# Optimization experiments

Measured on AMD Instinct MI355X. Metric: run time of the kernel, lower is better.

The kernel has to match this reference:

```python
import jax, jax.numpy as jnp
import numpy as np

B, S, D, V = 2, 4096, 2048, 32000
H, HD = 16, 128          # heads, head dim (H*HD == D)
BS = 16                  # block_size
N_ANCH = 128             # num_anchors (static: loss_mask=ones guarantees enough valid positions)
MASK_ID = 31999
DFF = 8192


def rms(x, w, eps=1e-6):
    return x * jax.lax.rsqrt(jnp.mean(x * x, axis=-1, keepdims=True) + eps) * w


def rope(x, pos):
    # x: (..., L, H, hd), pos: (..., L)
    hd = x.shape[-1]
    inv = 1.0 / (10000.0 ** (jnp.arange(0, hd, 2, dtype=jnp.float32) / hd))
    ang = pos[..., None, None].astype(jnp.float32) * inv  # (..., L, 1, hd/2)
    cos, sin = jnp.cos(ang), jnp.sin(ang)
    x1, x2 = x[..., : hd // 2], x[..., hd // 2 :]
    return jnp.concatenate([x1 * cos - x2 * sin, x2 * cos + x1 * sin], axis=-1).astype(x.dtype)


def setup_inputs() -> dict:
    key = jax.random.key(0)
    ks = jax.random.split(key, 12)
    s = 0.02
    return {
        "input_ids": jax.random.randint(ks[0], (B, S), 0, V, dtype=jnp.int32),
        "hidden_states": jax.random.normal(ks[1], (B, S, D), dtype=jnp.float32),
        "loss_mask": jnp.ones((B, S), dtype=jnp.float32),
        "rand_vals": jax.random.uniform(ks[2], (B, S - BS + 1), dtype=jnp.float32),
        "embed_table": jax.random.normal(ks[3], (V, D), dtype=jnp.float32) * s,
        "lm_head_w": jax.random.normal(ks[4], (V, D), dtype=jnp.float32) * s,
        "wq": jax.random.normal(ks[5], (D, D), dtype=jnp.float32) * s,
        "wk": jax.random.normal(ks[6], (D, D), dtype=jnp.float32) * s,
        "wv": jax.random.normal(ks[7], (D, D), dtype=jnp.float32) * s,
        "wo": jax.random.normal(ks[8], (D, D), dtype=jnp.float32) * s,
        "w_gate": jax.random.normal(ks[9], (D, DFF), dtype=jnp.float32) * s,
        "w_up": jax.random.normal(ks[10], (D, DFF), dtype=jnp.float32) * s,
        "w_down": jax.random.normal(ks[11], (DFF, D), dtype=jnp.float32) * s,
        "norm_attn": jnp.ones((D,), dtype=jnp.float32),
        "norm_mlp": jnp.ones((D,), dtype=jnp.float32),
        "norm_out": jnp.ones((D,), dtype=jnp.float32),
        "norm_chs": jnp.ones((D,), dtype=jnp.float32),
    }


def reference(input_ids, hidden_states, loss_mask, rand_vals, embed_table, lm_head_w,
              wq, wk, wv, wo, w_gate, w_up, w_down, norm_attn, norm_mlp, norm_out, norm_chs):
    max_anchor = S - BS
    # ---- anchor sampling: random permutation of valid positions via argsort of rand ----
    valid = loss_mask[:, : max_anchor + 1] > 0.5                       # (B, max_anchor+1)
    valid_counts = valid.sum(axis=1)
    idx = jnp.arange(max_anchor + 1, dtype=jnp.int32)
    masked_idx = jnp.where(valid, idx[None, :], S + 1)
    rv = jnp.where(valid, rand_vals, 2.0)
    order = jnp.argsort(rv, axis=1)
    gathered = jnp.take_along_axis(masked_idx, order, axis=1)
    anchors = jnp.sort(gathered[:, :N_ANCH], axis=1)                   # (B, N)
    keep = jnp.arange(N_ANCH)[None, :] < jnp.minimum(valid_counts, N_ANCH)[:, None]
    anchors = jnp.where(keep, anchors, 0)
    # ---- noise embedding: anchor token at block start, mask token elsewhere ----
    anchor_tok = jnp.take_along_axis(input_ids, jnp.clip(anchors, 0, S - 1), axis=1)
    first_tok = jnp.where(keep, anchor_tok, MASK_ID)
    noise_ids = jnp.full((B, N_ANCH, BS), MASK_ID, dtype=jnp.int32).at[:, :, 0].set(first_tok)
    x = embed_table[noise_ids]                                         # (B,N,BS,D)
    # ---- CHS context hidden: target hidden at anchor-1 ----
    ctx_pos = jnp.maximum(anchors - 1, 0)
    ctx = jnp.take_along_axis(hidden_states, ctx_pos[:, :, None], axis=1)  # (B,N,D)
    # ---- block-diagonal attention: per-block kv = [CHS_i | draft block i] (kv_len=1+BS) ----
    pos_q = anchors[:, :, None] + jnp.arange(BS)[None, None, :]        # (B,N,BS)
    pos_kv = jnp.concatenate([ctx_pos[:, :, None], pos_q], axis=2)     # (B,N,1+BS)
    hq = rms(x, norm_attn)
    hc = rms(ctx, norm_chs)[:, :, None, :]
    kv_in = jnp.concatenate([hc, hq], axis=2)                          # (B,N,1+BS,D)
    q = rope((hq @ wq).reshape(B, N_ANCH, BS, H, HD), pos_q)
    k = rope((kv_in @ wk).reshape(B, N_ANCH, 1 + BS, H, HD), pos_kv)
    v = (kv_in @ wv).reshape(B, N_ANCH, 1 + BS, H, HD)
    scores = jnp.einsum('bnqhd,bnkhd->bnhqk', q, k) * (1.0 / HD ** 0.5)
    attn = jax.nn.softmax(scores, axis=-1)
    out = jnp.einsum('bnhqk,bnkhd->bnqhd', attn, v).reshape(B, N_ANCH, BS, D) @ wo
    out = out * keep[:, :, None, None].astype(out.dtype)               # invalid blocks fully masked
    x = x + out
    h = rms(x, norm_mlp)
    x = x + (jax.nn.silu(h @ w_gate) * (h @ w_up)) @ w_down
    h_out = rms(x, norm_out)
    logits = h_out @ lm_head_w.T                                       # (B,N,BS,V)
    # ---- block-wise CE loss ----
    label_idx = anchors[:, :, None] + jnp.arange(BS)[None, None, :]
    valid_label = label_idx < S
    safe = jnp.minimum(label_idx, S - 1)
    targets = jnp.take_along_axis(jnp.broadcast_to(input_ids[:, None, :], (B, N_ANCH, S)), safe, axis=2)
    lm_g = jnp.take_along_axis(jnp.broadcast_to(loss_mask[:, None, :], (B, N_ANCH, S)), safe, axis=2)
    weight = (keep[:, :, None] & valid_label).astype(jnp.float32)
    weight = weight * (jnp.arange(BS) > 0)[None, None, :].astype(jnp.float32) * lm_g
    logp = jax.nn.log_softmax(logits, axis=-1)
    tok_logp = jnp.take_along_axis(logp, targets[..., None].astype(jnp.int32), axis=-1)[..., 0]
    loss = -(tok_logp * weight).sum() / (weight.sum() + 1e-6)
    pred = jnp.argmax(logits, axis=-1)
    accuracy = ((pred == targets) & (weight > 0.5)).sum().astype(jnp.float32) / (weight.sum() + 1e-6)
    return loss, accuracy
```

## Files before the change

kernel.cpp:

```cpp
#include <hip/hip_runtime.h>
#include <math.h>

typedef unsigned short u16;
typedef unsigned char u8;
typedef short v8s __attribute__((ext_vector_type(8)));
typedef u16   v4u __attribute__((ext_vector_type(4)));
typedef float v4f __attribute__((ext_vector_type(4)));
typedef int   v2i __attribute__((ext_vector_type(2)));
typedef int   v4i __attribute__((ext_vector_type(4)));

#define DEVFN static __device__ __forceinline__

constexpr int cB = 2, cS = 4096, cD = 2048, cV = 32000, cH = 16, cHD = 128;
constexpr int cBS = 16, cNA = 128, cMASK = 31999, cDFF = 8192;
constexpr int NCAND = cS - cBS + 1;
constexpr int MTOK  = cB * cNA * cBS;
constexpr int MKV   = cB * cNA * 17;
constexpr int NCH   = cV / 128;
constexpr int NCH2  = cV / 256;

constexpr int EPI_BF16 = 0, EPI_SILU = 1, EPI_OEMB = 2, EPI_DOWNACC = 3, EPI_STATS = 4;
constexpr int ASRC_BF16 = 0, ASRC_RMS = 1, ASRC_AOMAP = 2;

struct RmsSrc {
  const float* hs; const float* emb; const float* nattn; const float* nchs;
  const float* rowinv; const int* ftok; const int* cpos;
};

DEVFN u16 f2bf(float f) {
  union { float f; unsigned u; } a; a.f = f;
  unsigned u = a.u;
  u = u + 0x7fffu + ((u >> 16) & 1u);
  return (u16)(u >> 16);
}
DEVFN float bf2f(u16 h) {
  union { unsigned u; float f; } a; a.u = ((unsigned)h) << 16;
  return a.f;
}
DEVFN float waveSum(float v) {
  #pragma unroll
  for (int o = 32; o >= 1; o >>= 1) v += __shfl_xor(v, o);
  return v;
}
DEVFN void gload16(void* lds, const void* g) {
  __builtin_amdgcn_global_load_lds(
      (const __attribute__((address_space(1))) unsigned*)g,
      (__attribute__((address_space(3))) unsigned*)lds, 16, 0, 0);
}
DEVFN int pack4fp8(float a, float b, float c, float d) {
  int p = __builtin_amdgcn_cvt_pk_fp8_f32(a, b, 0, 0);
  p = __builtin_amdgcn_cvt_pk_fp8_f32(c, d, p, 1);
  return p;
}
DEVFN long perm8(long i) {
  return (i & ~63L) | (((i >> 3) & 3) << 4) | (((i >> 5) & 1) << 3);
}

__global__ void k_select(const float* __restrict__ lmask, const float* __restrict__ rv_in,
                         int* __restrict__ self) {
  int b = blockIdx.x >> 4, chunk = blockIdx.x & 15;
  __shared__ float rvs[4096];
  for (int i = threadIdx.x; i < NCAND; i += 256) {
    bool valid = lmask[(size_t)b * cS + i] > 0.5f;
    rvs[i] = valid ? rv_in[(size_t)b * NCAND + i] : 2.0f;
  }
  __syncthreads();
  int i = chunk * 256 + threadIdx.x;
  if (i < NCAND) {
    float v = rvs[i];
    int rank = 0;
    for (int j = 0; j < NCAND; ++j) {
      float u = rvs[j];
      rank += (u < v) || (u == v && j < i);
    }
    self[(size_t)b * NCAND + i] = (rank < cNA) ? 1 : 0;
  }
}

__global__ void k_anchors(const float* __restrict__ lmask, const int* __restrict__ self,
                          const int* __restrict__ ids, int* __restrict__ anchors,
                          int* __restrict__ keepA, int* __restrict__ ftok, int* __restrict__ cpos) {
  int b = blockIdx.x;
  __shared__ int flags[4096];
  __shared__ int ssum[256];
  __shared__ int soff[257];
  __shared__ int abuf[cNA];
  for (int i = threadIdx.x; i < 4096; i += 256)
    flags[i] = (i < NCAND) ? (self[(size_t)b * NCAND + i] && (lmask[(size_t)b * cS + i] > 0.5f)) : 0;
  if (threadIdx.x < cNA) abuf[threadIdx.x] = 0;
  __syncthreads();
  int s = 0;
  #pragma unroll
  for (int j = 0; j < 16; ++j) s += flags[threadIdx.x * 16 + j];
  ssum[threadIdx.x] = s;
  __syncthreads();
  if (threadIdx.x == 0) {
    int a = 0;
    for (int t = 0; t < 256; ++t) { soff[t] = a; a += ssum[t]; }
    soff[256] = a;
  }
  __syncthreads();
  int nsel = soff[256];
  int p = soff[threadIdx.x];
  for (int j = 0; j < 16; ++j) {
// ... 38 lines not shown
                         const int* __restrict__ ftok, const int* __restrict__ cpos,
                         u16* __restrict__ kv) {
  int r = blockIdx.x;
  int j = r % 17, bn = r / 17, b = bn >> 7;
  const float* src; const float* w;
  if (j == 0) { src = hs + ((size_t)b * cS + cpos[bn]) * cD; w = nchs; }
  else {
    int tok = (j == 1) ? ftok[bn] : cMASK;
    src = emb + (size_t)tok * cD; w = nattn;
  }
  float ss = 0.f;
  for (int d = threadIdx.x; d < cD; d += 256) { float v = src[d]; ss += v * v; }
  ss = waveSum(ss);
  __shared__ float red[4];
  if ((threadIdx.x & 63) == 0) red[threadIdx.x >> 6] = ss;
  __syncthreads();
  float tot = red[0] + red[1] + red[2] + red[3];
  float inv = 1.0f / sqrtf(tot / cD + 1e-6f);
  for (int d = threadIdx.x; d < cD; d += 256)
    kv[(size_t)r * cD + d] = f2bf(src[d] * inv * w[d]);
}

__global__ void k_rms(const float* __restrict__ xin, const float* __restrict__ w,
                      u16* __restrict__ outp) {
  int m = blockIdx.x;
  const float* row = xin + (size_t)m * cD;
  float ss = 0.f;
  for (int d = threadIdx.x; d < cD; d += 256) { float v = row[d]; ss += v * v; }
  ss = waveSum(ss);
  __shared__ float red[4];
  if ((threadIdx.x & 63) == 0) red[threadIdx.x >> 6] = ss;
  __syncthreads();
  float tot = red[0] + red[1] + red[2] + red[3];
  float inv = 1.0f / sqrtf(tot / cD + 1e-6f);
  for (int d = threadIdx.x; d < cD; d += 256)
    outp[(size_t)m * cD + d] = f2bf(row[d] * inv * w[d]);
}

__global__ void k_conv8(const float* __restrict__ in, u8* __restrict__ out, long n, float scale) {
  long i = ((long)blockIdx.x * 256 + threadIdx.x) * 8;
  long stride = (long)gridDim.x * 256 * 8;
  for (; i < n; i += stride) {
    v4f a = *(const v4f*)(in + i), b = *(const v4f*)(in + i + 4);
    v2i pk;
    pk[0] = pack4fp8(a[0] * scale, a[1] * scale, a[2] * scale, a[3] * scale);
    pk[1] = pack4fp8(b[0] * scale, b[1] * scale, b[2] * scale, b[3] * scale);
    *(v2i*)(out + perm8(i)) = pk;
  }
}

__global__ void k_cvt8(const u16* __restrict__ in, u8* __restrict__ out, long n) {
  long i = ((long)blockIdx.x * 256 + threadIdx.x) * 8;
  long stride = (long)gridDim.x * 256 * 8;
  for (; i < n; i += stride) {
    v8s a = *(const v8s*)(in + i);
    v2i pk;
    pk[0] = pack4fp8(bf2f((u16)a[0]), bf2f((u16)a[1]), bf2f((u16)a[2]), bf2f((u16)a[3]));
    pk[1] = pack4fp8(bf2f((u16)a[4]), bf2f((u16)a[5]), bf2f((u16)a[6]), bf2f((u16)a[7]));
    *(v2i*)(out + perm8(i)) = pk;
  }
}

__global__ void k_tconv(const float* __restrict__ W, u16* __restrict__ WT, int K, int N) {
  __shared__ u16 t[64][72];
  int n0 = blockIdx.x * 64, k0 = blockIdx.y * 64;
  int tid = threadIdx.x;
  int c4 = (tid & 15) * 4, r0 = tid >> 4;
  #pragma unroll
  for (int rr = 0; rr < 64; rr += 16) {
    int k = r0 + rr;
    v4f v = *(const v4f*)(W + (size_t)(k0 + k) * N + n0 + c4);
    #pragma unroll
    for (int e = 0; e < 4; ++e) t[c4 + e][k] = f2bf(v[e]);
  }
  __syncthreads();
  int n = tid >> 2, kq = (tid & 3) * 16;
  v8s o0, o1;
  #pragma unroll
  for (int e = 0; e < 8; ++e) { o0[e] = (short)t[n][kq + e]; o1[e] = (short)t[n][kq + 8 + e]; }
  *(v8s*)(WT + (size_t)(n0 + n) * K + k0 + kq) = o0;
  *(v8s*)(WT + (size_t)(n0 + n) * K + k0 + kq + 8) = o1;
}

template <int EPI>
__launch_bounds__(512, 1)
__global__ void k_gemm6(const u16* __restrict__ Abf, const u16* __restrict__ Bbf,
                        u16* __restrict__ Cbf, const u16* __restrict__ Gaux,
                        v4f* __restrict__ partials, int K, int ldc, int nch) {
  __shared__ __align__(16) u16 lds[65536];
  const int tid = threadIdx.x;
  const int lane = tid & 63, wid = tid >> 6;
  const int wm = wid >> 2, wn = wid & 3;
  const int lc = lane & 15, lq = lane >> 4;
  const int m0 = blockIdx.x * 256, n0 = blockIdx.y * 256;

  const u16* srcA[2]; const u16* srcB[2];
  #pragma unroll
  for (int i = 0; i < 2; ++i) {
    int s = i * 512 + tid;
    int row = s >> 2;
    int c2 = (s & 3) ^ ((row >> 1) & 3);
    srcA[i] = Abf + (size_t)(m0 + row) * K + c2 * 8;
    srcB[i] = Bbf + (size_t)(n0 + row) * K + c2 * 8;
  }

  v4f acc[8][4];
  #pragma unroll
  for (int i = 0; i < 8; ++i)
    #pragma unroll
    for (int j = 0; j < 4; ++j) acc[i][j] = (v4f){0.f, 0.f, 0.f, 0.f};

  const int fsw = lq ^ ((lc >> 1) & 3);
  int aoff[8], boff[4];
  #pragma unroll
  for (int mi = 0; mi < 8; ++mi) aoff[mi] = ((wm * 128 + mi * 16 + lc) * 4 + fsw) * 8;
  #pragma unroll
  for (int ni = 0; ni < 4; ++ni) boff[ni] = ((wn * 64 + ni * 16 + lc) * 4 + fsw) * 8;

  auto stageA = [&](int t, int kh) {
    int reg = (t & 1) * 32768 + kh * 8192;
    int koff = t * 64 + kh * 32;
    #pragma unroll
    for (int i = 0; i < 2; ++i)
      gload16(&lds[reg + i * 4096 + wid * 512], srcA[i] + koff);
  };
  auto stageB = [&](int t, int kh) {
    int reg = (t & 1) * 32768 + 16384 + kh * 8192;
    int koff = t * 64 + kh * 32;
    #pragma unroll
    for (int i = 0; i < 2; ++i)
      gload16(&lds[reg + i * 4096 + wid * 512], srcB[i] + koff);
  };

  stageA(0, 0); stageB(0, 0);
  stageA(0, 1); stageB(0, 1);
  stageA(1, 0); stageB(1, 0);
  asm volatile("s_waitcnt vmcnt(8)" ::: "memory");
  __builtin_amdgcn_s_barrier();

  const int NT = K >> 6;
  for (int t = 0; t < NT; ++t) {
    const int bufb = (t & 1) * 32768;
    const u16* Ab0 = &lds[bufb];
    const u16* Ab1 = &lds[bufb + 8192];
    const u16* Bb0 = &lds[bufb + 16384];
    const u16* Bb1 = &lds[bufb + 24576];
    v8s a_[4], b_[4];

    #pragma unroll
    for (int ni = 0; ni < 4; ++ni) b_[ni] = *(const v8s*)(Bb0 + boff[ni]);
    #pragma unroll
    for (int mi = 0; mi < 4; ++mi) a_[mi] = *(const v8s*)(Ab0 + aoff[mi]);
    if (t + 1 < NT) stageA(t + 1, 1);
    asm volatile("s_waitcnt lgkmcnt(0)" ::: "memory");
    __builtin_amdgcn_sched_barrier(0);
    __builtin_amdgcn_s_setprio(1);
    #pragma unroll
    for (int mi = 0; mi < 4; ++mi)
      #pragma unroll
      for (int ni = 0; ni < 4; ++ni)
        acc[mi][ni] = __builtin_amdgcn_mfma_f32_16x16x32_bf16(a_[mi], b_[ni], acc[mi][ni], 0, 0, 0);
    __builtin_amdgcn_s_setprio(0);
    __builtin_amdgcn_s_barrier();

    #pragma unroll
    for (int mi = 0; mi < 4; ++mi) a_[mi] = *(const v8s*)(Ab0 + aoff[mi + 4]);
    if (t + 1 < NT) stageB(t + 1, 1);
    asm volatile("s_waitcnt lgkmcnt(0)" ::: "memory");
    __builtin_amdgcn_sched_barrier(0);
    __builtin_amdgcn_s_setprio(1);
    #pragma unroll
    for (int mi = 0; mi < 4; ++mi)
      #pragma unroll
      for (int ni = 0; ni < 4; ++ni)
        acc[mi + 4][ni] = __builtin_amdgcn_mfma_f32_16x16x32_bf16(a_[mi], b_[ni], acc[mi + 4][ni], 0, 0, 0);
    __builtin_amdgcn_s_setprio(0);
    if (t + 1 < NT) { asm volatile("s_waitcnt vmcnt(4)" ::: "memory"); }
    else            { asm volatile("s_waitcnt vmcnt(0)" ::: "memory"); }
    __builtin_amdgcn_s_barrier();

    #pragma unroll
    for (int ni = 0; ni < 4; ++ni) b_[ni] = *(const v8s*)(Bb1 + boff[ni]);
    #pragma unroll
    for (int mi = 0; mi < 4; ++mi) a_[mi] = *(const v8s*)(Ab1 + aoff[mi]);
    if (t + 2 < NT) stageA(t + 2, 0);
    asm volatile("s_waitcnt lgkmcnt(0)" ::: "memory");
    __builtin_amdgcn_sched_barrier(0);
    __builtin_amdgcn_s_setprio(1);
    #pragma unroll
    for (int mi = 0; mi < 4; ++mi)
      #pragma unroll
      for (int ni = 0; ni < 4; ++ni)
        acc[mi][ni] = __builtin_amdgcn_mfma_f32_16x16x32_bf16(a_[mi], b_[ni], acc[mi][ni], 0, 0, 0);
    __builtin_amdgcn_s_setprio(0);
    __builtin_amdgcn_s_barrier();

    #pragma unroll
    for (int mi = 0; mi < 4; ++mi) a_[mi] = *(const v8s*)(Ab1 + aoff[mi + 4]);
    if (t + 2 < NT) stageB(t + 2, 0);
    asm volatile("s_waitcnt lgkmcnt(0)" ::: "memory");
    __builtin_amdgcn_sched_barrier(0);
    __builtin_amdgcn_s_setprio(1);
    #pragma unroll
    for (int mi = 0; mi < 4; ++mi)
      #pragma unroll
      for (int ni = 0; ni < 4; ++ni)
        acc[mi + 4][ni] = __builtin_amdgcn_mfma_f32_16x16x32_bf16(a_[mi], b_[ni], acc[mi + 4][ni], 0, 0, 0);
    __builtin_amdgcn_s_setprio(0);
    __builtin_amdgcn_s_barrier();
  }
  asm volatile("s_waitcnt vmcnt(0)" ::: "memory");

  #pragma unroll
  for (int mi = 0; mi < 8; ++mi)
    #pragma unroll
    for (int ni = 0; ni < 4; ++ni)
      #pragma unroll
      for (int r = 0; r < 4; ++r) {
        int grow = m0 + wm * 128 + mi * 16 + lq * 4 + r;
        int gcol = n0 + wn * 64 + ni * 16 + lc;
        size_t idx = (size_t)grow * ldc + gcol;
        float vv = acc[mi][ni][r];
        if constexpr (EPI == EPI_BF16) {
          Cbf[idx] = f2bf(vv);
        } else {
          float g = bf2f(Gaux[idx]);
          Cbf[idx] = f2bf(vv * g / (1.0f + __expf(-g)));
        }
      }
  (void)partials; (void)nch;
}

__launch_bounds__(512, 2)
__global__ void k_gemm8(const u8* __restrict__ A8, const u8* __restrict__ B8,
                        v4f* __restrict__ partials, int K, int nch) {
  __shared__ __align__(16) u8 lds8[65536];
  const int tid = threadIdx.x;
  const int lane = tid & 63, wid = tid >> 6;
  const int wm = wid >> 2, wn = wid & 3;
  const int lc = lane & 15, lq = lane >> 4;
  const int m0 = blockIdx.x * 256, n0 = blockIdx.y * 256;

  const u8* srcA[2]; const u8* srcB[2];
  #pragma unroll
  for (int i = 0; i < 2; ++i) {
    int ci = i * 512 + tid;
    int r = ci >> 2;
    int logc = (ci & 3) ^ ((r >> 1) & 3);
    srcA[i] = A8 + (size_t)(m0 + r) * K + logc * 16;
    srcB[i] = B8 + (size_t)(n0 + r) * K + logc * 16;
  }

  v4f acc[8][4];
  #pragma unroll
  for (int i = 0; i < 8; ++i)
    #pragma unroll
    for (int j = 0; j < 4; ++j) acc[i][j] = (v4f){0.f, 0.f, 0.f, 0.f};

  const int csw = (lc >> 1) & 3;
  int aoff[8], boff[4];
  #pragma unroll
  for (int mi = 0; mi < 8; ++mi) aoff[mi] = (wm * 128 + mi * 16 + lc) * 64 + ((lq ^ csw) << 4);
  #pragma unroll
  for (int ni = 0; ni < 4; ++ni) boff[ni] = (wn * 64 + ni * 16 + lc) * 64 + ((lq ^ csw) << 4);

  auto stageA = [&](int t, int i) {
    gload16(&lds8[(t & 1) * 32768 + i * 8192 + wid * 1024], srcA[i] + t * 64);
  };
  auto stageB = [&](int t, int i) {
    gload16(&lds8[(t & 1) * 32768 + 16384 + i * 8192 + wid * 1024], srcB[i] + t * 64);
  };

  stageA(0, 0); stageA(0, 1); stageB(0, 0); stageB(0, 1);
  stageA(1, 0); stageA(1, 1); stageB(1, 0); stageB(1, 1);
  asm volatile("s_waitcnt vmcnt(4)" ::: "memory");
  __builtin_amdgcn_s_barrier();

  union Frag { v4i v; long long ll[2]; };
  const int NT = K >> 6;
  for (int t = 0; t < NT; ++t) {
    const u8* Ab = &lds8[(t & 1) * 32768];
    const u8* Bb = Ab + 16384;
    Frag fa[8], fb[4];

    #pragma unroll
    for (int ni = 0; ni < 4; ++ni) fb[ni].v = *(const v4i*)(Bb + boff[ni]);
    #pragma unroll
    for (int mi = 0; mi < 4; ++mi) fa[mi].v = *(const v4i*)(Ab + aoff[mi]);
    asm volatile("s_waitcnt lgkmcnt(0)" ::: "memory");
    __builtin_amdgcn_sched_barrier(0);
    __builtin_amdgcn_s_setprio(1);
    #pragma unroll
    for (int mi = 0; mi < 4; ++mi)
      #pragma unroll
      for (int ni = 0; ni < 4; ++ni)
        acc[mi][ni] = __builtin_amdgcn_mfma_f32_16x16x32_fp8_fp8(fa[mi].ll[0], fb[ni].ll[0], acc[mi][ni], 0, 0, 0);
    __builtin_amdgcn_s_setprio(0);
    __builtin_amdgcn_s_barrier();

    #pragma unroll
    for (int mi = 0; mi < 4; ++mi) fa[mi + 4].v = *(const v4i*)(Ab + aoff[mi + 4]);
    if (t + 2 < NT) stageB(t + 2, 0);
    asm volatile("s_waitcnt lgkmcnt(0)" ::: "memory");
    __builtin_amdgcn_sched_barrier(0);
    __builtin_amdgcn_s_setprio(1);
    #pragma unroll
    for (int mi = 0; mi < 4; ++mi)
      #pragma unroll
      for (int ni = 0; ni < 4; ++ni)
        acc[mi + 4][ni] = __builtin_amdgcn_mfma_f32_16x16x32_fp8_fp8(fa[mi + 4].ll[0], fb[ni].ll[0], acc[mi + 4][ni], 0, 0, 0);
    __builtin_amdgcn_s_setprio(0);
    __builtin_amdgcn_s_barrier();

    if (t + 2 < NT) { stageB(t + 2, 1); stageA(t + 2, 0); }
    __builtin_amdgcn_s_setprio(1);
    #pragma unroll
    for (int mi = 0; mi < 4; ++mi)
      #pragma unroll
      for (int ni = 0; ni < 4; ++ni)
        acc[mi][ni] = __builtin_amdgcn_mfma_f32_16x16x32_fp8_fp8(fa[mi].ll[1], fb[ni].ll[1], acc[mi][ni], 0, 0, 0);
    __builtin_amdgcn_s_setprio(0);
    __builtin_amdgcn_s_barrier();

    if (t + 2 < NT) stageA(t + 2, 1);
    __builtin_amdgcn_s_setprio(1);
    #pragma unroll
    for (int mi = 0; mi < 4; ++mi)
      #pragma unroll
      for (int ni = 0; ni < 4; ++ni)
        acc[mi + 4][ni] = __builtin_amdgcn_mfma_f32_16x16x32_fp8_fp8(fa[mi + 4].ll[1], fb[ni].ll[1], acc[mi + 4][ni], 0, 0, 0);
    __builtin_amdgcn_s_setprio(0);
    if (t + 2 < NT) { asm volatile("s_waitcnt vmcnt(4)" ::: "memory"); }
    else            { asm volatile("s_waitcnt vmcnt(0)" ::: "memory"); }
    __builtin_amdgcn_s_barrier();
  }
  asm volatile("s_waitcnt vmcnt(0)" ::: "memory");

  #pragma unroll
  for (int mi = 0; mi < 8; ++mi)
    #pragma unroll
    for (int ni = 0; ni < 4; ++ni)
      acc[mi][ni] *= 0.015625f;

  float* s_mx = (float*)lds8;
  float* s_sm = (float*)(lds8 + 4096);
  int*   s_ax = (int*)(lds8 + 8192);
  __syncthreads();
  #pragma unroll
  for (int mi = 0; mi < 8; ++mi) {
    #pragma unroll
    for (int r = 0; r < 4; ++r) {
      float v0 = acc[mi][0][r], v1 = acc[mi][1][r], v2 = acc[mi][2][r], v3 = acc[mi][3][r];
      float mx = v0; int ax = lc;
      if (v1 > mx) { mx = v1; ax = 16 + lc; }
      if (v2 > mx) { mx = v2; ax = 32 + lc; }
      if (v3 > mx) { mx = v3; ax = 48 + lc; }
      #pragma unroll
      for (int off = 1; off < 16; off <<= 1) {
        float om = __shfl_xor(mx, off); int oa = __shfl_xor(ax, off);
        if (om > mx || (om == mx && oa < ax)) { mx = om; ax = oa; }
      }
      float se = __expf(v0 - mx) + __expf(v1 - mx) + __expf(v2 - mx) + __expf(v3 - mx);
      #pragma unroll
      for (int off = 1; off < 16; off <<= 1) se += __shfl_xor(se, off);
      if (lc == 0) {
        int row = wm * 128 + mi * 16 + lq * 4 + r;
        s_mx[row * 4 + wn] = mx; s_sm[row * 4 + wn] = se; s_ax[row * 4 + wn] = wn * 64 + ax;
      }
    }
  }
  __syncthreads();
  if (tid < 256) {
    float gm = s_mx[tid * 4]; int ga = s_ax[tid * 4];
    #pragma unroll
    for (int w = 1; w < 4; ++w) {
      float m = s_mx[tid * 4 + w];
      if (m > gm) { gm = m; ga = s_ax[tid * 4 + w]; }
    }
    float gs = 0.f;
    #pragma unroll
    for (int w = 0; w < 4; ++w) gs += s_sm[tid * 4 + w] * __expf(s_mx[tid * 4 + w] - gm);
    v4f rec; rec[0] = gm; rec[1] = gs; rec[2] = __int_as_float(n0 + ga); rec[3] = 0.f;
    partials[(size_t)(m0 + tid) * nch + blockIdx.y] = rec;
  }
}

template <int ASRC, int EPI>
__launch_bounds__(256, 2)
__global__ void k_gemm4(const u16* __restrict__ Abf, const u16* __restrict__ Bbf,
                        u16* __restrict__ Cbf, float* __restrict__ Cf32,
                        const int* __restrict__ keepArr, RmsSrc rs, int K, int ldb, int ldc) {
  __shared__ __align__(16) u16 lds[2][16384];
  const int tid = threadIdx.x;
  const int lane = tid & 63, wid = tid >> 6;
  const int wm = wid >> 1, wn = wid & 1;
  const int lc = lane & 15, lq = lane >> 4;
  const int m0 = blockIdx.x * 128, n0 = blockIdx.y * 128;

  const u16* srcA[4]; const u16* srcB[4];
  #pragma unroll
  for (int i = 0; i < 4; ++i) {
    int s = i * 256 + tid;
    int row = s >> 3;
    int c3 = (s & 7) ^ (row & 7);
    int ar = m0 + row;
    if constexpr (ASRC == ASRC_AOMAP) ar = (ar >> 4) * 17 + 1 + (ar & 15);
    srcA[i] = Abf + (size_t)ar * K + c3 * 8;
    srcB[i] = Bbf + (size_t)(n0 + row) * ldb + c3 * 8;
  }

  v4f acc[4][4];
  #pragma unroll
  for (int i = 0; i < 4; ++i)
    #pragma unroll
    for (int j = 0; j < 4; ++j) acc[i][j] = (v4f){0.f, 0.f, 0.f, 0.f};

  const int sw = lc & 7;
  const int aoff0 = (((wm * 64 + lc) * 8 + 0 + lq) ^ sw) * 8;
  const int aoff1 = (((wm * 64 + lc) * 8 + 4 + lq) ^ sw) * 8;
  const int boff0 = (((wn * 64 + lc) * 8 + 0 + lq) ^ sw) * 8;
  const int boff1 = (((wn * 64 + lc) * 8 + 4 + lq) ^ sw) * 8;

  auto stageTo = [&](int b) {
    u16* dA = &lds[b][0] + wid * 512;
    u16* dB = &lds[b][8192] + wid * 512;
    #pragma unroll
    for (int i = 0; i < 4; ++i) { gload16(dA + i * 2048, srcA[i]); srcA[i] += 64; }
    #pragma unroll
    for (int i = 0; i < 4; ++i) { gload16(dB + i * 2048, srcB[i]); srcB[i] += 64; }
  };

  stageTo(0);
  const int NT = K >> 6;
  for (int t = 0; t < NT; ++t) {
    const int cur = t & 1;
    if (t + 1 < NT) {
      stageTo(cur ^ 1);
      asm volatile("s_waitcnt vmcnt(8)" ::: "memory");
    } else {
      asm volatile("s_waitcnt vmcnt(0)" ::: "memory");
    }
    __builtin_amdgcn_s_barrier();
    const u16* Ab = &lds[cur][0];
    const u16* Bb = &lds[cur][8192];
    v8s a0[4], a1[4], b0[4], b1[4];
    #pragma unroll
    for (int mi = 0; mi < 4; ++mi) a0[mi] = *(const v8s*)(Ab + aoff0 + mi * 1024);
    #pragma unroll
    for (int ni = 0; ni < 4; ++ni) b0[ni] = *(const v8s*)(Bb + boff0 + ni * 1024);
    #pragma unroll
    for (int mi = 0; mi < 4; ++mi) a1[mi] = *(const v8s*)(Ab + aoff1 + mi * 1024);
    #pragma unroll
    for (int ni = 0; ni < 4; ++ni) b1[ni] = *(const v8s*)(Bb + boff1 + ni * 1024);
    __builtin_amdgcn_s_setprio(1);
    #pragma unroll
    for (int mi = 0; mi < 4; ++mi)
      #pragma unroll
      for (int ni = 0; ni < 4; ++ni)
        acc[mi][ni] = __builtin_amdgcn_mfma_f32_16x16x32_bf16(a0[mi], b0[ni], acc[mi][ni], 0, 0, 0);
    __builtin_amdgcn_s_setprio(0);
    asm volatile("s_waitcnt lgkmcnt(0)" ::: "memory");
    __builtin_amdgcn_sched_barrier(0);
    __builtin_amdgcn_s_barrier();
    __builtin_amdgcn_s_setprio(1);
    #pragma unroll
    for (int mi = 0; mi < 4; ++mi)
// ... 328 lines not shown
__global__ void k_heartbeat(float* outp) {
  if (threadIdx.x == 0) { outp[0] = -55.0f; outp[1] = -55.0f; }
}
__global__ void k_sentinel(float* outp) {
  if (threadIdx.x == 0) { outp[0] = -777.0f; outp[1] = -777.0f; }
}

extern "C" void kernel_launch(void* const* d_in, const int* in_sizes, int n_in,
                              void* d_out, int out_size, void* d_ws, size_t ws_size,
                              hipStream_t stream) {
  const int*   ids   = (const int*)  d_in[0];
  const float* hs    = (const float*)d_in[1];
  const float* lmask = (const float*)d_in[2];
  const float* rv    = (const float*)d_in[3];
  const float* emb   = (const float*)d_in[4];
  const float* wlm   = (const float*)d_in[5];
  const float* wq    = (const float*)d_in[6];
  const float* wk    = (const float*)d_in[7];
  const float* wv    = (const float*)d_in[8];
  const float* wo    = (const float*)d_in[9];
  const float* wg    = (const float*)d_in[10];
  const float* wu    = (const float*)d_in[11];
  const float* wd    = (const float*)d_in[12];
  const float* nattn = (const float*)d_in[13];
  const float* nmlp  = (const float*)d_in[14];
  const float* nout  = (const float*)d_in[15];
  const float* nchs  = (const float*)d_in[16];
  (void)in_sizes; (void)n_in; (void)out_size;

  float* outp = (float*)d_out;
  k_heartbeat<<<dim3(1), 64, 0, stream>>>(outp);

  char* wsb = (char*)d_ws;
  size_t off = 0;
  auto alloc = [&](size_t bytes) -> void* {
    void* p = wsb + off;
    off = (off + bytes + 255) & ~(size_t)255;
    return p;
  };
  int*   anchors = (int*)  alloc((size_t)cB * cNA * 4);
  int*   keepA   = (int*)  alloc((size_t)cB * cNA * 4);
  int*   ftok    = (int*)  alloc((size_t)cB * cNA * 4);
  int*   cpos    = (int*)  alloc((size_t)cB * cNA * 4);
  int*   self    = (int*)  alloc((size_t)cB * NCAND * 4);
  float* rowinv  = (float*)alloc((size_t)MKV * 4);
  int*   ttok    = (int*)  alloc((size_t)MTOK * 4);
  float* tlogit  = (float*)alloc((size_t)MTOK * 4);
  float* tokOut  = (float*)alloc((size_t)MTOK * 4 * 4);

  const size_t szQ  = (size_t)MKV * cD * 2;
  const size_t szX  = (size_t)MTOK * cD * 4;
  u16* qb = (u16*)alloc(szQ);
  const size_t a1off = off;

  RmsSrc rs{hs, emb, nattn, nchs, rowinv, ftok, cpos};

  k_select <<<dim3(cB * 16), 256, 0, stream>>>(lmask, rv, self);
  k_anchors<<<dim3(cB),      256, 0, stream>>>(lmask, self, ids, anchors, keepA, ftok, cpos);

  const size_t szKV   = szQ;
  const size_t szCbuf = (size_t)MTOK * 4096 * 2;
  size_t kvb_off  = a1off;
  size_t a1f_off  = (kvb_off + szKV + 255) & ~(size_t)255;
  size_t a1f_sz   = 2 * szQ > (szX + szCbuf) ? 2 * szQ : (szX + szCbuf);
  size_t wreg_off = (a1f_off + a1f_sz + 255) & ~(size_t)255;
  size_t wreg_sz  = (size_t)cV * cD * 2;
  size_t need_fast = wreg_off + wreg_sz;

  if (need_fast <= ws_size) {
    u16*   kvb   = (u16*)(wsb + kvb_off);
    u16*   kb    = (u16*)(wsb + a1f_off);
    u16*   vb    = (u16*)(wsb + a1f_off + szQ);
    float* xb    = (float*)(wsb + a1f_off);
    u16*   cbuf  = (u16*)(wsb + a1f_off + szX);
    v4f*   parts = (v4f*)(wsb + a1f_off);
    u8*    h8    = (u8*)(wsb + a1f_off + (size_t)16 * 1024 * 1024);
    u16*   hb    = qb;
    u16*   houtb = qb;
    u16*   wT    = (u16*)(wsb + wreg_off);
    const size_t szDD = (size_t)cD * cD;
    u16* wqT = wT;            u16* wkT = wT + szDD;
    u16* wvT = wT + 2 * szDD; u16* woT = wT + 3 * szDD;
    const size_t szDF = (size_t)cD * cDFF;
    u16* wgT = wT; u16* wuT = wT + szDF; u16* wdT = wT + 2 * szDF;
    u8*  wlm8 = (u8*)wT;

    k_build2<<<dim3(MKV), 256, 0, stream>>>(hs, emb, nattn, nchs, ftok, cpos, kvb);

    k_tconv<<<dim3(32, 32), 256, 0, stream>>>(wq, wqT, cD, cD);
    k_tconv<<<dim3(32, 32), 256, 0, stream>>>(wk, wkT, cD, cD);
    k_tconv<<<dim3(32, 32), 256, 0, stream>>>(wv, wvT, cD, cD);
    k_tconv<<<dim3(32, 32), 256, 0, stream>>>(wo, woT, cD, cD);

    k_gemm4<ASRC_BF16, EPI_BF16><<<dim3(MKV / 128, cD / 128), 256, 0, stream>>>(
        kvb, wqT, qb, nullptr, nullptr, rs, cD, cD, cD);
    k_gemm4<ASRC_BF16, EPI_BF16><<<dim3(MKV / 128, cD / 128), 256, 0, stream>>>(
        kvb, wkT, kb, nullptr, nullptr, rs, cD, cD, cD);
    k_gemm4<ASRC_BF16, EPI_BF16><<<dim3(MKV / 128, cD / 128), 256, 0, stream>>>(
        kvb, wvT, vb, nullptr, nullptr, rs, cD, cD, cD);

    k_rope<<<dim3(2 * MKV), 256, 0, stream>>>(qb, kb, anchors, cpos);
    k_attn<<<dim3(cB * cNA * cH), 64, 0, stream>>>(qb, kb, vb);

    k_gemm4<ASRC_AOMAP, EPI_OEMB><<<dim3(MTOK / 128, cD / 128), 256, 0, stream>>>(
        qb, woT, nullptr, xb, keepA, rs, cD, cD, cD);

    k_rms<<<dim3(MTOK), 256, 0, stream>>>(xb, nmlp, hb);

    k_tconv<<<dim3(128, 32), 256, 0, stream>>>(wg, wgT, cD, cDFF);
    k_tconv<<<dim3(128, 32), 256, 0, stream>>>(wu, wuT, cD, cDFF);
    k_tconv<<<dim3(32, 128), 256, 0, stream>>>(wd, wdT, cDFF, cD);

    for (int cb = 0; cb < cDFF; cb += 4096) {
      k_gemm6<EPI_BF16><<<dim3(MTOK / 256, 16), 512, 0, stream>>>(
          hb, wgT + (size_t)cb * cD, cbuf, nullptr, nullptr, cD, 4096, 0);
      k_gemm6<EPI_SILU><<<dim3(MTOK / 256, 16), 512, 0, stream>>>(
          hb, wuT + (size_t)cb * cD, cbuf, cbuf, nullptr, cD, 4096, 0);
      k_gemm4<ASRC_BF16, EPI_DOWNACC><<<dim3(MTOK / 128, cD / 128), 256, 0, stream>>>(
          cbuf, wdT + cb, nullptr, xb, nullptr, rs, 4096, cDFF, cD);
    }

    k_rms<<<dim3(MTOK), 256, 0, stream>>>(xb, nout, houtb);

    k_tgt<<<dim3(MTOK / 4), 256, 0, stream>>>(houtb, wlm, ids, anchors, ttok, tlogit);

    k_cvt8 <<<dim3(1024), 256, 0, stream>>>(houtb, h8, (long)MTOK * cD);
    k_conv8<<<dim3(2048), 256, 0, stream>>>(wlm, wlm8, (long)cV * cD, 64.0f);
    k_gemm8<<<dim3(MTOK / 256, NCH2), 512, 0, stream>>>(h8, wlm8, parts, cD, NCH2);

    k_combine<<<dim3(MTOK), 256, 0, stream>>>(parts, ttok, tlogit, keepA, anchors, lmask, tokOut, NCH2);
    k_final  <<<dim3(1), 256, 0, stream>>>(tokOut, outp);
    return;
  }

  const int cwopts[4] = {4096, 2048, 1024, 512};
  int CW = 0;
  for (int ci = 0; ci < 4; ++ci) {
    int cw = cwopts[ci];
    size_t cbufsz = (size_t)MTOK * cw * 2;
    size_t s1 = 2 * szQ;
    size_t s2 = szX + cbufsz;
    size_t sz = s1 > s2 ? s1 : s2;
    size_t pmin = (size_t)MTOK * NCH * 16;
    if (pmin > sz) sz = pmin;
    if (a1off + sz <= ws_size) { CW = cw; break; }
  }
  if (CW == 0) { k_sentinel<<<dim3(1), 64, 0, stream>>>(outp); return; }

  u16*   kb    = (u16*)(wsb + a1off);
  u16*   vb    = (u16*)(wsb + a1off + szQ);
  float* xb    = (float*)(wsb + a1off);
  u16*   cbuf  = (u16*)(wsb + a1off + szX);
  v4f*   parts = (v4f*)(wsb + a1off);
  u16*   hb    = qb;
  u16*   houtb = qb;

  k_rowinv<<<dim3(MKV), 256, 0, stream>>>(hs, emb, ftok, cpos, rowinv);

  k_gemm<ASRC_RMS, 0, EPI_BF16><<<dim3(MKV / 128, cD / 128), 256, 0, stream>>>(
      nullptr, wq, qb, nullptr, nullptr, nullptr, nullptr, rs, cD, cD, cD);
  k_gemm<ASRC_RMS, 0, EPI_BF16><<<dim3(MKV / 128, cD / 128), 256, 0, stream>>>(
      nullptr, wk, kb, nullptr, nullptr, nullptr, nullptr, rs, cD, cD, cD);
  k_gemm<ASRC_RMS, 0, EPI_BF16><<<dim3(MKV / 128, cD / 128), 256, 0, stream>>>(
      nullptr, wv, vb, nullptr, nullptr, nullptr, nullptr, rs, cD, cD, cD);

  k_rope<<<dim3(2 * MKV), 256, 0, stream>>>(qb, kb, anchors, cpos);
  k_attn<<<dim3(cB * cNA * cH), 64, 0, stream>>>(qb, kb, vb);

  k_gemm<ASRC_AOMAP, 0, EPI_OEMB><<<dim3(MTOK / 128, cD / 128), 256, 0, stream>>>(
      qb, wo, nullptr, xb, nullptr, keepA, nullptr, rs, cD, cD, cD);

  k_rms<<<dim3(MTOK), 256, 0, stream>>>(xb, nmlp, hb);

  for (int cb = 0; cb < cDFF; cb += CW) {
    k_gemm<ASRC_BF16, 0, EPI_BF16><<<dim3(MTOK / 128, CW / 128), 256, 0, stream>>>(
        hb, wg + cb, cbuf, nullptr, nullptr, nullptr, nullptr, rs, cD, cDFF, CW);
    k_gemm<ASRC_BF16, 0, EPI_SILU><<<dim3(MTOK / 128, CW / 128), 256, 0, stream>>>(
        hb, wu + cb, cbuf, nullptr, cbuf, nullptr, nullptr, rs, cD, cDFF, CW);
    k_gemm<ASRC_BF16, 0, EPI_DOWNACC><<<dim3(MTOK / 128, cD / 128), 256, 0, stream>>>(
        cbuf, wd + (size_t)cb * cD, nullptr, xb, nullptr, nullptr, nullptr, rs, CW, cD, cD);
  }

  k_rms<<<dim3(MTOK), 256, 0, stream>>>(xb, nout, houtb);

  k_tgt<<<dim3(MTOK / 4), 256, 0, stream>>>(houtb, wlm, ids, anchors, ttok, tlogit);
  k_gemm<ASRC_BF16, 1, EPI_STATS><<<dim3(MTOK / 128, cV / 128), 256, 0, stream>>>(
      houtb, wlm, nullptr, nullptr, nullptr, nullptr, parts, rs, cD, cD, 0);

  k_combine<<<dim3(MTOK), 256, 0, stream>>>(parts, ttok, tlogit, keepA, anchors, lmask, tokOut, NCH);
  k_final  <<<dim3(1), 256, 0, stream>>>(tokOut, outp);
}
```

Baseline: 1.557 ms.

## Fuse gate/up GEMMs via interleaved weights and triple-buffer fp8 LM-head GEMM

```diff
diff --git a/kernel.cpp b/kernel.cpp
--- a/kernel.cpp
+++ b/kernel.cpp
@@ -19,7 +19,7 @@
 constexpr int NCH   = cV / 128;
 constexpr int NCH2  = cV / 256;
 
-constexpr int EPI_BF16 = 0, EPI_SILU = 1, EPI_OEMB = 2, EPI_DOWNACC = 3, EPI_STATS = 4;
+constexpr int EPI_BF16 = 0, EPI_SILU = 1, EPI_OEMB = 2, EPI_DOWNACC = 3, EPI_STATS = 4, EPI_GLU = 5;
 constexpr int ASRC_BF16 = 0, ASRC_RMS = 1, ASRC_AOMAP = 2;
 
 struct RmsSrc {
@@ -224,6 +224,29 @@
   *(v8s*)(WT + (size_t)(n0 + n) * K + k0 + kq + 8) = o1;
 }
 
+__global__ void k_tconv2(const float* __restrict__ W, u16* __restrict__ WT, int K, int N, int goff) {
+  __shared__ u16 t[64][72];
+  int n0 = blockIdx.x * 64, k0 = blockIdx.y * 64;
+  int tid = threadIdx.x;
+  int c4 = (tid & 15) * 4, r0 = tid >> 4;
+  #pragma unroll
+  for (int rr = 0; rr < 64; rr += 16) {
+    int k = r0 + rr;
+    v4f v = *(const v4f*)(W + (size_t)(k0 + k) * N + n0 + c4);
+    #pragma unroll
+    for (int e = 0; e < 4; ++e) t[c4 + e][k] = f2bf(v[e]);
+  }
+  __syncthreads();
+  int n = tid >> 2, kq = (tid & 3) * 16;
+  int gn = n0 + n;
+  size_t rout = ((size_t)(gn >> 4) << 5) + goff + (gn & 15);
+  v8s o0, o1;
+  #pragma unroll
+  for (int e = 0; e < 8; ++e) { o0[e] = (short)t[n][kq + e]; o1[e] = (short)t[n][kq + 8 + e]; }
+  *(v8s*)(WT + rout * K + k0 + kq) = o0;
+  *(v8s*)(WT + rout * K + k0 + kq + 8) = o1;
+}
+
 template <int EPI>
 __launch_bounds__(512, 1)
 __global__ void k_gemm6(const u16* __restrict__ Abf, const u16* __restrict__ Bbf,
@@ -353,30 +376,45 @@
   }
   asm volatile("s_waitcnt vmcnt(0)" ::: "memory");
 
-  #pragma unroll
-  for (int mi = 0; mi < 8; ++mi)
-    #pragma unroll
-    for (int ni = 0; ni < 4; ++ni)
-      #pragma unroll
-      for (int r = 0; r < 4; ++r) {
-        int grow = m0 + wm * 128 + mi * 16 + lq * 4 + r;
-        int gcol = n0 + wn * 64 + ni * 16 + lc;
-        size_t idx = (size_t)grow * ldc + gcol;
-        float vv = acc[mi][ni][r];
-        if constexpr (EPI == EPI_BF16) {
-          Cbf[idx] = f2bf(vv);
-        } else {
-          float g = bf2f(Gaux[idx]);
-          Cbf[idx] = f2bf(vv * g / (1.0f + __expf(-g)));
+  if constexpr (EPI == EPI_GLU) {
+    #pragma unroll
+    for (int mi = 0; mi < 8; ++mi)
+      #pragma unroll
+      for (int np = 0; np < 2; ++np)
+        #pragma unroll
+        for (int r = 0; r < 4; ++r) {
+          int grow = m0 + wm * 128 + mi * 16 + lq * 4 + r;
+          int gcol = (n0 >> 1) + wn * 32 + np * 16 + lc;
+          float g = acc[mi][2 * np][r];
+          float u = acc[mi][2 * np + 1][r];
+          Cbf[(size_t)grow * ldc + gcol] = f2bf(u * g / (1.0f + __expf(-g)));
         }
-      }
+  } else {
+    #pragma unroll
+    for (int mi = 0; mi < 8; ++mi)
+      #pragma unroll
+      for (int ni = 0; ni < 4; ++ni)
+        #pragma unroll
+        for (int r = 0; r < 4; ++r) {
+          int grow = m0 + wm * 128 + mi * 16 + lq * 4 + r;
+          int gcol = n0 + wn * 64 + ni * 16 + lc;
+          size_t idx = (size_t)grow * ldc + gcol;
+          float vv = acc[mi][ni][r];
+          if constexpr (EPI == EPI_BF16) {
+            Cbf[idx] = f2bf(vv);
+          } else {
+            float g = bf2f(Gaux[idx]);
+            Cbf[idx] = f2bf(vv * g / (1.0f + __expf(-g)));
+          }
+        }
+  }
   (void)partials; (void)nch;
 }
 
-__launch_bounds__(512, 2)
+__launch_bounds__(512, 1)
 __global__ void k_gemm8(const u8* __restrict__ A8, const u8* __restrict__ B8,
                         v4f* __restrict__ partials, int K, int nch) {
-  __shared__ __align__(16) u8 lds8[65536];
+  __shared__ __align__(16) u8 lds8[98304];
   const int tid = threadIdx.x;
   const int lane = tid & 63, wid = tid >> 6;
   const int wm = wid >> 2, wn = wid & 3;
@@ -406,22 +444,24 @@
   #pragma unroll
   for (int ni = 0; ni < 4; ++ni) boff[ni] = (wn * 64 + ni * 16 + lc) * 64 + ((lq ^ csw) << 4);
 
-  auto stageA = [&](int t, int i) {
-    gload16(&lds8[(t & 1) * 32768 + i * 8192 + wid * 1024], srcA[i] + t * 64);
+  auto stageA = [&](int buf, int t, int i) {
+    gload16(&lds8[buf * 32768 + i * 8192 + wid * 1024], srcA[i] + t * 64);
   };
-  auto stageB = [&](int t, int i) {
-    gload16(&lds8[(t & 1) * 32768 + 16384 + i * 8192 + wid * 1024], srcB[i] + t * 64);
+  auto stageB = [&](int buf, int t, int i) {
+    gload16(&lds8[buf * 32768 + 16384 + i * 8192 + wid * 1024], srcB[i] + t * 64);
   };
 
-  stageA(0, 0); stageA(0, 1); stageB(0, 0); stageB(0, 1);
-  stageA(1, 0); stageA(1, 1); stageB(1, 0); stageB(1, 1);
-  asm volatile("s_waitcnt vmcnt(4)" ::: "memory");
+  stageA(0, 0, 0); stageA(0, 0, 1); stageB(0, 0, 0); stageB(0, 0, 1);
+  stageA(1, 1, 0); stageA(1, 1, 1); stageB(1, 1, 0); stageB(1, 1, 1);
+  stageA(2, 2, 0); stageA(2, 2, 1); stageB(2, 2, 0); stageB(2, 2, 1);
+  asm volatile("s_waitcnt vmcnt(8)" ::: "memory");
   __builtin_amdgcn_s_barrier();
 
   union Frag { v4i v; long long ll[2]; };
   const int NT = K >> 6;
+  int cur = 0;
   for (int t = 0; t < NT; ++t) {
-    const u8* Ab = &lds8[(t & 1) * 32768];
+    const u8* Ab = &lds8[cur * 32768];
     const u8* Bb = Ab + 16384;
     Frag fa[8], fb[4];
 
@@ -442,7 +482,7 @@
 
     #pragma unroll
     for (int mi = 0; mi < 4; ++mi) fa[mi + 4].v = *(const v4i*)(Ab + aoff[mi + 4]);
-    if (t + 2 < NT) stageB(t + 2, 0);
+    if (t + 3 < NT) stageB(cur, t + 3, 0);
     asm volatile("s_waitcnt lgkmcnt(0)" ::: "memory");
     __builtin_amdgcn_sched_barrier(0);
     __builtin_amdgcn_s_setprio(1);
@@ -454,7 +494,7 @@
     __builtin_amdgcn_s_setprio(0);
     __builtin_amdgcn_s_barrier();
 
-    if (t + 2 < NT) { stageB(t + 2, 1); stageA(t + 2, 0); }
+    if (t + 3 < NT) { stageB(cur, t + 3, 1); stageA(cur, t + 3, 0); }
     __builtin_amdgcn_s_setprio(1);
     #pragma unroll
     for (int mi = 0; mi < 4; ++mi)
@@ -464,7 +504,7 @@
     __builtin_amdgcn_s_setprio(0);
     __builtin_amdgcn_s_barrier();
 
-    if (t + 2 < NT) stageA(t + 2, 1);
+    if (t + 3 < NT) stageA(cur, t + 3, 1);
     __builtin_amdgcn_s_setprio(1);
     #pragma unroll
     for (int mi = 0; mi < 4; ++mi)
@@ -472,9 +512,10 @@
       for (int ni = 0; ni < 4; ++ni)
         acc[mi + 4][ni] = __builtin_amdgcn_mfma_f32_16x16x32_fp8_fp8(fa[mi + 4].ll[1], fb[ni].ll[1], acc[mi + 4][ni], 0, 0, 0);
     __builtin_amdgcn_s_setprio(0);
-    if (t + 2 < NT) { asm volatile("s_waitcnt vmcnt(4)" ::: "memory"); }
+    if (t + 3 < NT) { asm volatile("s_waitcnt vmcnt(8)" ::: "memory"); }
     else            { asm volatile("s_waitcnt vmcnt(0)" ::: "memory"); }
     __builtin_amdgcn_s_barrier();
+    cur = (cur == 2) ? 0 : cur + 1;
   }
   asm volatile("s_waitcnt vmcnt(0)" ::: "memory");
 
@@ -1018,7 +1059,8 @@
     u16* wqT = wT;            u16* wkT = wT + szDD;
     u16* wvT = wT + 2 * szDD; u16* woT = wT + 3 * szDD;
     const size_t szDF = (size_t)cD * cDFF;
-    u16* wgT = wT; u16* wuT = wT + szDF; u16* wdT = wT + 2 * szDF;
+    u16* wguT = wT;
+    u16* wdT  = wT + 2 * szDF;
     u8*  wlm8 = (u8*)wT;
 
     k_build2<<<dim3(MKV), 256, 0, stream>>>(hs, emb, nattn, nchs, ftok, cpos, kvb);
@@ -1043,15 +1085,13 @@
 
     k_rms<<<dim3(MTOK), 256, 0, stream>>>(xb, nmlp, hb);
 
-    k_tconv<<<dim3(128, 32), 256, 0, stream>>>(wg, wgT, cD, cDFF);
-    k_tconv<<<dim3(128, 32), 256, 0, stream>>>(wu, wuT, cD, cDFF);
-    k_tconv<<<dim3(32, 128), 256, 0, stream>>>(wd, wdT, cDFF, cD);
+    k_tconv2<<<dim3(128, 32), 256, 0, stream>>>(wg, wguT, cD, cDFF, 0);
+    k_tconv2<<<dim3(128, 32), 256, 0, stream>>>(wu, wguT, cD, cDFF, 16);
+    k_tconv <<<dim3(32, 128), 256, 0, stream>>>(wd, wdT, cDFF, cD);
 
     for (int cb = 0; cb < cDFF; cb += 4096) {
-      k_gemm6<EPI_BF16><<<dim3(MTOK / 256, 16), 512, 0, stream>>>(
-          hb, wgT + (size_t)cb * cD, cbuf, nullptr, nullptr, cD, 4096, 0);
-      k_gemm6<EPI_SILU><<<dim3(MTOK / 256, 16), 512, 0, stream>>>(
-          hb, wuT + (size_t)cb * cD, cbuf, cbuf, nullptr, cD, 4096, 0);
+      k_gemm6<EPI_GLU><<<dim3(MTOK / 256, 32), 512, 0, stream>>>(
+          hb, wguT + (size_t)cb * 2 * cD, cbuf, nullptr, nullptr, cD, 4096, 0);
       k_gemm4<ASRC_BF16, EPI_DOWNACC><<<dim3(MTOK / 128, cD / 128), 256, 0, stream>>>(
           cbuf, wdT + cb, nullptr, xb, nullptr, rs, 4096, cDFF, cD);
     }
```

Result: no change. 1.545 ms (-0.7%).

## Fuse gate/up projections into one FP8 GEMM with SwiGLU epilogue

Applied to the files above, without the earlier changes.

```diff
diff --git a/kernel.cpp b/kernel.cpp
--- a/kernel.cpp
+++ b/kernel.cpp
@@ -19,7 +19,7 @@
 constexpr int NCH   = cV / 128;
 constexpr int NCH2  = cV / 256;
 
-constexpr int EPI_BF16 = 0, EPI_SILU = 1, EPI_OEMB = 2, EPI_DOWNACC = 3, EPI_STATS = 4;
+constexpr int EPI_BF16 = 0, EPI_SILU = 1, EPI_OEMB = 2, EPI_DOWNACC = 3, EPI_STATS = 4, EPI_GLU = 5;
 constexpr int ASRC_BF16 = 0, ASRC_RMS = 1, ASRC_AOMAP = 2;
 
 struct RmsSrc {
@@ -224,6 +224,33 @@
   *(v8s*)(WT + (size_t)(n0 + n) * K + k0 + kq + 8) = o1;
 }
 
+__global__ void k_tconv8(const float* __restrict__ W, u8* __restrict__ WT8,
+                         int K, int N, int goff, float scale) {
+  __shared__ float tf[64][65];
+  int n0 = blockIdx.x * 64, k0 = blockIdx.y * 64;
+  int tid = threadIdx.x;
+  int c4 = (tid & 15) * 4, r0 = tid >> 4;
+  #pragma unroll
+  for (int rr = 0; rr < 64; rr += 16) {
+    int k = r0 + rr;
+    v4f v = *(const v4f*)(W + (size_t)(k0 + k) * N + n0 + c4);
+    #pragma unroll
+    for (int e = 0; e < 4; ++e) tf[c4 + e][k] = v[e];
+  }
+  __syncthreads();
+  int n = tid >> 2, kq = (tid & 3) * 16;
+  int gn = n0 + n;
+  size_t rout = ((size_t)(gn >> 4) << 5) + goff + (gn & 15);
+  long base = (long)rout * K + k0 + kq;
+  v2i p0, p1;
+  p0[0] = pack4fp8(tf[n][kq + 0] * scale, tf[n][kq + 1] * scale, tf[n][kq + 2] * scale, tf[n][kq + 3] * scale);
+  p0[1] = pack4fp8(tf[n][kq + 4] * scale, tf[n][kq + 5] * scale, tf[n][kq + 6] * scale, tf[n][kq + 7] * scale);
+  p1[0] = pack4fp8(tf[n][kq + 8] * scale, tf[n][kq + 9] * scale, tf[n][kq + 10] * scale, tf[n][kq + 11] * scale);
+  p1[1] = pack4fp8(tf[n][kq + 12] * scale, tf[n][kq + 13] * scale, tf[n][kq + 14] * scale, tf[n][kq + 15] * scale);
+  *(v2i*)(WT8 + perm8(base)) = p0;
+  *(v2i*)(WT8 + perm8(base + 8)) = p1;
+}
+
 template <int EPI>
 __launch_bounds__(512, 1)
 __global__ void k_gemm6(const u16* __restrict__ Abf, const u16* __restrict__ Bbf,
@@ -353,29 +380,46 @@
   }
   asm volatile("s_waitcnt vmcnt(0)" ::: "memory");
 
-  #pragma unroll
-  for (int mi = 0; mi < 8; ++mi)
-    #pragma unroll
-    for (int ni = 0; ni < 4; ++ni)
-      #pragma unroll
-      for (int r = 0; r < 4; ++r) {
-        int grow = m0 + wm * 128 + mi * 16 + lq * 4 + r;
-        int gcol = n0 + wn * 64 + ni * 16 + lc;
-        size_t idx = (size_t)grow * ldc + gcol;
-        float vv = acc[mi][ni][r];
-        if constexpr (EPI == EPI_BF16) {
-          Cbf[idx] = f2bf(vv);
-        } else {
-          float g = bf2f(Gaux[idx]);
-          Cbf[idx] = f2bf(vv * g / (1.0f + __expf(-g)));
+  if constexpr (EPI == EPI_GLU) {
+    #pragma unroll
+    for (int mi = 0; mi < 8; ++mi)
+      #pragma unroll
+      for (int np = 0; np < 2; ++np)
+        #pragma unroll
+        for (int r = 0; r < 4; ++r) {
+          int grow = m0 + wm * 128 + mi * 16 + lq * 4 + r;
+          int gcol = (n0 >> 1) + wn * 32 + np * 16 + lc;
+          float g = acc[mi][2 * np][r];
+          float u = acc[mi][2 * np + 1][r];
+          Cbf[(size_t)grow * ldc + gcol] = f2bf(u * g / (1.0f + __expf(-g)));
         }
-      }
+  } else {
+    #pragma unroll
+    for (int mi = 0; mi < 8; ++mi)
+      #pragma unroll
+      for (int ni = 0; ni < 4; ++ni)
+        #pragma unroll
+        for (int r = 0; r < 4; ++r) {
+          int grow = m0 + wm * 128 + mi * 16 + lq * 4 + r;
+          int gcol = n0 + wn * 64 + ni * 16 + lc;
+          size_t idx = (size_t)grow * ldc + gcol;
+          float vv = acc[mi][ni][r];
+          if constexpr (EPI == EPI_BF16) {
+            Cbf[idx] = f2bf(vv);
+          } else {
+            float g = bf2f(Gaux[idx]);
+            Cbf[idx] = f2bf(vv * g / (1.0f + __expf(-g)));
+          }
+        }
+  }
   (void)partials; (void)nch;
 }
 
+template <int EPI>
 __launch_bounds__(512, 2)
 __global__ void k_gemm8(const u8* __restrict__ A8, const u8* __restrict__ B8,
-                        v4f* __restrict__ partials, int K, int nch) {
+                        u16* __restrict__ Cbf, v4f* __restrict__ partials,
+                        int K, int ldc, int nch) {
   __shared__ __align__(16) u8 lds8[65536];
   const int tid = threadIdx.x;
   const int lane = tid & 63, wid = tid >> 6;
@@ -484,46 +528,62 @@
     for (int ni = 0; ni < 4; ++ni)
       acc[mi][ni] *= 0.015625f;
 
-  float* s_mx = (float*)lds8;
-  float* s_sm = (float*)(lds8 + 4096);
-  int*   s_ax = (int*)(lds8 + 8192);
-  __syncthreads();
-  #pragma unroll
-  for (int mi = 0; mi < 8; ++mi) {
-    #pragma unroll
-    for (int r = 0; r < 4; ++r) {
-      float v0 = acc[mi][0][r], v1 = acc[mi][1][r], v2 = acc[mi][2][r], v3 = acc[mi][3][r];
-      float mx = v0; int ax = lc;
-      if (v1 > mx) { mx = v1; ax = 16 + lc; }
-      if (v2 > mx) { mx = v2; ax = 32 + lc; }
-      if (v3 > mx) { mx = v3; ax = 48 + lc; }
-      #pragma unroll
-      for (int off = 1; off < 16; off <<= 1) {
-        float om = __shfl_xor(mx, off); int oa = __shfl_xor(ax, off);
-        if (om > mx || (om == mx && oa < ax)) { mx = om; ax = oa; }
-      }
-      float se = __expf(v0 - mx) + __expf(v1 - mx) + __expf(v2 - mx) + __expf(v3 - mx);
-      #pragma unroll
-      for (int off = 1; off < 16; off <<= 1) se += __shfl_xor(se, off);
-      if (lc == 0) {
-        int row = wm * 128 + mi * 16 + lq * 4 + r;
-        s_mx[row * 4 + wn] = mx; s_sm[row * 4 + wn] = se; s_ax[row * 4 + wn] = wn * 64 + ax;
+  if constexpr (EPI == EPI_GLU) {
+    #pragma unroll
+    for (int mi = 0; mi < 8; ++mi)
+      #pragma unroll
+      for (int np = 0; np < 2; ++np)
+        #pragma unroll
+        for (int r = 0; r < 4; ++r) {
+          int grow = m0 + wm * 128 + mi * 16 + lq * 4 + r;
+          int gcol = (n0 >> 1) + wn * 32 + np * 16 + lc;
+          float g = acc[mi][2 * np][r];
+          float u = acc[mi][2 * np + 1][r];
+          Cbf[(size_t)grow * ldc + gcol] = f2bf(u * g / (1.0f + __expf(-g)));
+        }
+    return;
+  } else {
+    float* s_mx = (float*)lds8;
+    float* s_sm = (float*)(lds8 + 4096);
+    int*   s_ax = (int*)(lds8 + 8192);
+    __syncthreads();
+    #pragma unroll
+    for (int mi = 0; mi < 8; ++mi) {
+      #pragma unroll
+      for (int r = 0; r < 4; ++r) {
+        float v0 = acc[mi][0][r], v1 = acc[mi][1][r], v2 = acc[mi][2][r], v3 = acc[mi][3][r];
+        float mx = v0; int ax = lc;
+        if (v1 > mx) { mx = v1; ax = 16 + lc; }
+        if (v2 > mx) { mx = v2; ax = 32 + lc; }
+        if (v3 > mx) { mx = v3; ax = 48 + lc; }
+        #pragma unroll
+        for (int off = 1; off < 16; off <<= 1) {
+          float om = __shfl_xor(mx, off); int oa = __shfl_xor(ax, off);
+          if (om > mx || (om == mx && oa < ax)) { mx = om; ax = oa; }
+        }
+        float se = __expf(v0 - mx) + __expf(v1 - mx) + __expf(v2 - mx) + __expf(v3 - mx);
+        #pragma unroll
+        for (int off = 1; off < 16; off <<= 1) se += __shfl_xor(se, off);
+        if (lc == 0) {
+          int row = wm * 128 + mi * 16 + lq * 4 + r;
+          s_mx[row * 4 + wn] = mx; s_sm[row * 4 + wn] = se; s_ax[row * 4 + wn] = wn * 64 + ax;
+        }
       }
     }
-  }
-  __syncthreads();
-  if (tid < 256) {
-    float gm = s_mx[tid * 4]; int ga = s_ax[tid * 4];
-    #pragma unroll
-    for (int w = 1; w < 4; ++w) {
-      float m = s_mx[tid * 4 + w];
-      if (m > gm) { gm = m; ga = s_ax[tid * 4 + w]; }
+    __syncthreads();
+    if (tid < 256) {
+      float gm = s_mx[tid * 4]; int ga = s_ax[tid * 4];
+      #pragma unroll
+      for (int w = 1; w < 4; ++w) {
+        float m = s_mx[tid * 4 + w];
+        if (m > gm) { gm = m; ga = s_ax[tid * 4 + w]; }
+      }
+      float gs = 0.f;
+      #pragma unroll
+      for (int w = 0; w < 4; ++w) gs += s_sm[tid * 4 + w] * __expf(s_mx[tid * 4 + w] - gm);
+      v4f rec; rec[0] = gm; rec[1] = gs; rec[2] = __int_as_float(n0 + ga); rec[3] = 0.f;
+      partials[(size_t)(m0 + tid) * nch + blockIdx.y] = rec;
     }
-    float gs = 0.f;
-    #pragma unroll
-    for (int w = 0; w < 4; ++w) gs += s_sm[tid * 4 + w] * __expf(s_mx[tid * 4 + w] - gm);
-    v4f rec; rec[0] = gm; rec[1] = gs; rec[2] = __int_as_float(n0 + ga); rec[3] = 0.f;
-    partials[(size_t)(m0 + tid) * nch + blockIdx.y] = rec;
   }
 }
 
@@ -1018,7 +1078,9 @@
     u16* wqT = wT;            u16* wkT = wT + szDD;
     u16* wvT = wT + 2 * szDD; u16* woT = wT + 3 * szDD;
     const size_t szDF = (size_t)cD * cDFF;
-    u16* wgT = wT; u16* wuT = wT + szDF; u16* wdT = wT + 2 * szDF;
+    u8*  wgu8 = (u8*)wT;
+    u16* wdT  = wT + 2 * szDF;
+    u8*  h8m  = (u8*)(wT + 3 * szDF);
     u8*  wlm8 = (u8*)wT;
 
     k_build2<<<dim3(MKV), 256, 0, stream>>>(hs, emb, nattn, nchs, ftok, cpos, kvb);
@@ -1042,16 +1104,15 @@
         qb, woT, nullptr, xb, keepA, rs, cD, cD, cD);
 
     k_rms<<<dim3(MTOK), 256, 0, stream>>>(xb, nmlp, hb);
-
-    k_tconv<<<dim3(128, 32), 256, 0, stream>>>(wg, wgT, cD, cDFF);
-    k_tconv<<<dim3(128, 32), 256, 0, stream>>>(wu, wuT, cD, cDFF);
-    k_tconv<<<dim3(32, 128), 256, 0, stream>>>(wd, wdT, cDFF, cD);
+    k_cvt8<<<dim3(1024), 256, 0, stream>>>(hb, h8m, (long)MTOK * cD);
+
+    k_tconv8<<<dim3(128, 32), 256, 0, stream>>>(wg, wgu8, cD, cDFF, 0, 64.0f);
+    k_tconv8<<<dim3(128, 32), 256, 0, stream>>>(wu, wgu8, cD, cDFF, 16, 64.0f);
+    k_tconv <<<dim3(32, 128), 256, 0, stream>>>(wd, wdT, cDFF, cD);
 
     for (int cb = 0; cb < cDFF; cb += 4096) {
-      k_gemm6<EPI_BF16><<<dim3(MTOK / 256, 16), 512, 0, stream>>>(
-          hb, wgT + (size_t)cb * cD, cbuf, nullptr, nullptr, cD, 4096, 0);
-      k_gemm6<EPI_SILU><<<dim3(MTOK / 256, 16), 512, 0, stream>>>(
-          hb, wuT + (size_t)cb * cD, cbuf, cbuf, nullptr, cD, 4096, 0);
+      k_gemm8<EPI_GLU><<<dim3(MTOK / 256, 32), 512, 0, stream>>>(
+          h8m, wgu8 + (size_t)cb * 2 * cD, cbuf, nullptr, cD, 4096, 0);
       k_gemm4<ASRC_BF16, EPI_DOWNACC><<<dim3(MTOK / 128, cD / 128), 256, 0, stream>>>(
           cbuf, wdT + cb, nullptr, xb, nullptr, rs, 4096, cDFF, cD);
     }
@@ -1062,7 +1123,8 @@
 
     k_cvt8 <<<dim3(1024), 256, 0, stream>>>(houtb, h8, (long)MTOK * cD);
     k_conv8<<<dim3(2048), 256, 0, stream>>>(wlm, wlm8, (long)cV * cD, 64.0f);
-    k_gemm8<<<dim3(MTOK / 256, NCH2), 512, 0, stream>>>(h8, wlm8, parts, cD, NCH2);
+    k_gemm8<EPI_STATS><<<dim3(MTOK / 256, NCH2), 512, 0, stream>>>(
+        h8, wlm8, nullptr, parts, cD, 0, NCH2);
 
     k_combine<<<dim3(MTOK), 256, 0, stream>>>(parts, ttok, tlogit, keepA, anchors, lmask, tokOut, NCH2);
     k_final  <<<dim3(1), 256, 0, stream>>>(tokOut, outp);
```

Result: faster. 1.497 ms (-3.8%).
